# Performance work log

Measured on AMD Instinct MI355X. Metric: run time of the kernel, lower is better.

Reference implementation:

```python
import jax, jax.numpy as jnp
import numpy as np

N_WIN = 7    # n_win hardcoded in AR_Attention
TOPK = 4     # topk routing windows
HEADS = 8    # num_heads


def setup_inputs() -> dict:
    key = jax.random.key(0)
    ks = jax.random.split(key, 6)
    B, H, W, C = 4, 56, 56, 256
    s = 0.02
    x = jax.random.normal(ks[0], (B, H, W, C), jnp.float32)
    Wqkv = jax.random.normal(ks[1], (C, 3 * C), jnp.float32) * s  # Linear(dim, 3*dim) (qk_dim=dim)
    bqkv = jnp.zeros((3 * C,), jnp.float32)
    Wo = jax.random.normal(ks[2], (C, C), jnp.float32) * s        # output projection Linear(dim, dim)
    bo = jnp.zeros((C,), jnp.float32)
    lepe_w = jax.random.normal(ks[3], (5, 5, 1, C), jnp.float32) * s  # 5x5 depthwise conv (side_dwconv=5)
    lepe_b = jnp.zeros((C,), jnp.float32)
    return {"x": x, "Wqkv": Wqkv, "bqkv": bqkv, "Wo": Wo, "bo": bo,
            "lepe_w": lepe_w, "lepe_b": lepe_b}


def reference(x, Wqkv, bqkv, Wo, bo, lepe_w, lepe_b):
    B, H, W, C = x.shape
    nw = N_WIN
    h, w = H // nw, W // nw           # region size (8x8)
    p2 = nw * nw                      # number of regions (49)
    hd = C // HEADS                   # head dim
    scale = float(C) ** -0.5          # qk_scale = qk_dim ** -0.5 (qk_dim = dim)

    # region partition: [B,H,W,C] -> [B,p2,h,w,C]
    xr = x.reshape(B, nw, h, nw, w, C).transpose(0, 1, 3, 2, 4, 5).reshape(B, p2, h, w, C)

    qkv = xr @ Wqkv + bqkv            # [B,p2,h,w,3C]
    q, kv = qkv[..., :C], qkv[..., C:]

    q_pix = q.reshape(B, p2, h * w, C)
    kv_pix = kv.reshape(B, p2, h * w, 2 * C)   # kv_downsample_mode='identity'

    # region-level queries/keys via per-window mean pooling
    q_win = q.mean((2, 3))                     # [B,p2,C]
    k_win = kv[..., :C].mean((2, 3))           # [B,p2,C]

    # LEPE: 5x5 depthwise conv on v over the full image grid
    v_img = kv[..., C:].reshape(B, nw, nw, h, w, C).transpose(0, 1, 3, 2, 4, 5).reshape(B, H, W, C)
    lepe = jax.lax.conv_general_dilated(
        v_img, lepe_w, (1, 1), 'SAME',
        dimension_numbers=('NHWC', 'HWIO', 'NHWC'),
        feature_group_count=C) + lepe_b

    # top-k window routing (param_routing=False, hard routing, mul_weight='none')
    r_logit = jnp.einsum('bpc,bqc->bpq', q_win * scale, k_win)  # [B,p2,p2]
    _, r_idx = jax.lax.top_k(r_logit, TOPK)                     # [B,p2,TOPK]

    # gather selected kv windows: [B,p2,TOPK,h*w,2C]
    kv_sel = jax.vmap(lambda kvp, i: kvp[i])(kv_pix, r_idx)

    k_sel = kv_sel[..., :C].reshape(B, p2, TOPK * h * w, HEADS, hd)
    v_sel = kv_sel[..., C:].reshape(B, p2, TOPK * h * w, HEADS, hd)
    qh = q_pix.reshape(B, p2, h * w, HEADS, hd)

    attn = jnp.einsum('bpqnd,bpknd->bpnqk', qh * scale, k_sel)  # [B,p2,heads,hw,TOPK*hw]
    attn = jax.nn.softmax(attn, axis=-1)
    out = jnp.einsum('bpnqk,bpknd->bpqnd', attn, v_sel).reshape(B, p2, h, w, C)

    # windows back to image grid
    out = out.reshape(B, nw, nw, h, w, C).transpose(0, 1, 3, 2, 4, 5).reshape(B, H, W, C)
    out = out + lepe
    return out @ Wo + bo
```

## Files before the change

### kernel.cpp

```cpp
#include <hip/hip_runtime.h>
#include <hip/hip_bf16.h>

#define NPIX 12544

typedef short bf16x8 __attribute__((ext_vector_type(8)));
typedef float f32x4  __attribute__((ext_vector_type(4)));

__device__ __forceinline__ float bf2f(unsigned short u) {
    unsigned int x = ((unsigned int)u) << 16;
    float f; __builtin_memcpy(&f, &x, sizeof(f)); return f;
}
__device__ __forceinline__ unsigned short f2bf(float f) {
    __hip_bfloat16 h = __float2bfloat16(f);
    unsigned short u; __builtin_memcpy(&u, &h, 2); return u;
}
__device__ __forceinline__ void load_lds16(const unsigned short* g, unsigned short* l) {
    __builtin_amdgcn_global_load_lds(
        (const __attribute__((address_space(1))) unsigned int*)g,
        (__attribute__((address_space(3))) unsigned int*)l,
        16, 0, 0);
}

__global__ __launch_bounds__(256) void k_prep(
    const float* __restrict__ X, unsigned short* __restrict__ Xb,
    float* __restrict__ xmean,
    const float* __restrict__ Wqkv, const float* __restrict__ Wo,
    unsigned short* __restrict__ Wtq, unsigned short* __restrict__ Wto)
{
    __shared__ __align__(16) unsigned char sm[64 * 65 * 4];
    const int t = threadIdx.x;
    const int blk = blockIdx.x;
    if (blk < 392) {
        float* part = (float*)sm;
        const int w = blk >> 1, hc = blk & 1;
        const int b = w / 49, p = w % 49;
        const int wi = p / 7, wj = p % 7;
        const int ch0 = hc * 128;
        const int ps = t >> 5, cg = t & 31;
        float4 s = {0.f, 0.f, 0.f, 0.f};
        #pragma unroll
        for (int i = 0; i < 8; i++) {
            int pp = ps * 8 + i;
            int y = wi * 8 + (pp >> 3), x = wj * 8 + (pp & 7);
            int idx = (((b * 56) + y) * 56 + x) * 256 + ch0 + cg * 4;
            float4 v = *reinterpret_cast<const float4*>(X + idx);
            s.x += v.x; s.y += v.y; s.z += v.z; s.w += v.w;
            ushort4 o = { f2bf(v.x), f2bf(v.y), f2bf(v.z), f2bf(v.w) };
            *reinterpret_cast<ushort4*>(Xb + idx) = o;
        }
        *reinterpret_cast<float4*>(part + t * 4) = *reinterpret_cast<float4*>(&s);
        __syncthreads();
        if (t < 32) {
            float4 m = {0.f, 0.f, 0.f, 0.f};
            #pragma unroll
            for (int ps2 = 0; ps2 < 8; ps2++) {
                float4 v = *reinterpret_cast<float4*>(part + (ps2 * 32 + t) * 4);
                m.x += v.x; m.y += v.y; m.z += v.z; m.w += v.w;
            }
            m.x *= (1.f / 64.f); m.y *= (1.f / 64.f);
            m.z *= (1.f / 64.f); m.w *= (1.f / 64.f);
            *reinterpret_cast<float4*>(xmean + w * 256 + ch0 + t * 4) = m;
        }
    } else {
        float* tile = (float*)sm;
        int tb = blk - 392;
        const float* Wsrc; unsigned short* Wdst; int N, kt, nt;
        if (tb < 48) { Wsrc = Wqkv; Wdst = Wtq; N = 768; kt = tb / 12; nt = tb % 12; }
        else { tb -= 48; Wsrc = Wo; Wdst = Wto; N = 256; kt = tb / 4; nt = tb % 4; }
        const int k0 = kt * 64, n0 = nt * 64;
        const int r0 = t >> 6, c = t & 63;
        #pragma unroll
        for (int i = 0; i < 16; i++) {
            int r = i * 4 + r0;
            tile[r * 65 + c] = Wsrc[(size_t)(k0 + r) * N + n0 + c];
        }
        __syncthreads();
        #pragma unroll
        for (int i = 0; i < 16; i++) {
            int n = i * 4 + r0;
            Wdst[(size_t)(n0 + n) * 256 + k0 + c] = f2bf(tile[c * 65 + n]);
        }
    }
}

__global__ __launch_bounds__(256) void k_main1(
    const unsigned short* __restrict__ A,
    const unsigned short* __restrict__ Bt,
    const float* __restrict__ bias,
    unsigned short* __restrict__ O,
    const float* __restrict__ xmean,
    const float* __restrict__ Wqkv,
    float* __restrict__ qwin, float* __restrict__ kwin)
{
    __shared__ __align__(16) unsigned char sm1[16384];
    const int t = threadIdx.x;
    const int blk = blockIdx.x;
    if (blk < 588) {
        unsigned short* As = (unsigned short*)sm1;
        unsigned short* Bs = (unsigned short*)(sm1 + 8192);
        const int m0 = (blk % 98) * 128, n0 = (blk / 98) * 128;
        const int wave = t >> 6, lane = t & 63, quad = lane >> 4, lo = lane & 15;
        const int wm = wave & 1, wn = wave >> 1;
        const int sr = wave * 16 + (lane >> 2);
        const int sc = lane & 3;
        f32x4 acc[4][4];
        #pragma unroll
        for (int i = 0; i < 4; i++)
            #pragma unroll
            for (int j = 0; j < 4; j++) acc[i][j] = (f32x4){0.f, 0.f, 0.f, 0.f};

        for (int kt = 0; kt < 256; kt += 32) {
            __syncthreads();
            #pragma unroll
            for (int j = 0; j < 2; j++) {
                int row = j * 64 + sr;
                int e = sc ^ ((row >> 1) & 3);
                load_lds16(A  + (size_t)(m0 + row) * 256 + kt + e * 8, &As[row * 32 + sc * 8]);
                load_lds16(Bt + (size_t)(n0 + row) * 256 + kt + e * 8, &Bs[row * 32 + sc * 8]);
            }
            __syncthreads();
            bf16x8 af[4], bfr[4];
            #pragma unroll
            for (int mt = 0; mt < 4; mt++) {
                int row = wm * 64 + mt * 16 + lo;
                int c = quad ^ ((row >> 1) & 3);
                af[mt] = *reinterpret_cast<const bf16x8*>(&As[row * 32 + c * 8]);
            }
            #pragma unroll
            for (int nt = 0; nt < 4; nt++) {
                int col = wn * 64 + nt * 16 + lo;
                int c = quad ^ ((col >> 1) & 3);
                bfr[nt] = *reinterpret_cast<const bf16x8*>(&Bs[col * 32 + c * 8]);
            }
            #pragma unroll
            for (int mt = 0; mt < 4; mt++)
                #pragma unroll
                for (int nt = 0; nt < 4; nt++)
                    acc[mt][nt] = __builtin_amdgcn_mfma_f32_16x16x32_bf16(
                        af[mt], bfr[nt], acc[mt][nt], 0, 0, 0);
        }
        float bv[4];
        #pragma unroll
        for (int nt = 0; nt < 4; nt++) bv[nt] = bias[n0 + wn * 64 + nt * 16 + lo];
        #pragma unroll
        for (int mt = 0; mt < 4; mt++)
            #pragma unroll
            for (int nt = 0; nt < 4; nt++) {
                int n = n0 + wn * 64 + nt * 16 + lo;
                #pragma unroll
                for (int r = 0; r < 4; r++) {
                    int m = m0 + wm * 64 + mt * 16 + quad * 4 + r;
                    O[m * 768 + n] = f2bf(acc[mt][nt][r] + bv[nt]);
                }
            }
    } else {
        float* xs = (float*)sm1;
        const int u = blk - 588;
        const int bp = u % 196;
        const int half = u / 196;
        const int c = t;
        xs[c] = xmean[bp * 256 + c];
        __syncthreads();
        const int col = half * 256 + c;
        float a = 0.f;
        for (int k = 0; k < 256; k++) a += xs[k] * Wqkv[k * 768 + col];
        float* outp = half ? kwin : qwin;
        outp[bp * 256 + c] = a + bias[col];
    }
}

__global__ __launch_bounds__(256) void k_main2(
    const float* __restrict__ qwin, const float* __restrict__ kwin,
    int* __restrict__ ridx,
    const unsigned short* __restrict__ QKV,
    const float* __restrict__ lw, const float* __restrict__ lb,
    unsigned short* __restrict__ Olepe)
{
    __shared__ __align__(16) unsigned char sm2[25600];
    const int t = threadIdx.x;
    const int blk = blockIdx.x;
    if (blk < 196) {
        float* part = (float*)sm2;
        float* lg   = (float*)(sm2 + 49 * 4 * 4);
        const int b = blk / 49, p = blk % 49;
        if (t < 196) {
            int d = t >> 2, pr = t & 3;
            const float* qp = &qwin[(b * 49 + p) * 256];
            const float* kp = &kwin[(b * 49 + d) * 256];
            float a = 0.f;
            for (int ch = pr * 64; ch < pr * 64 + 64; ch++) a += qp[ch] * kp[ch];
            part[d * 4 + pr] = a;
        }
        __syncthreads();
        if (t < 49) lg[t] = part[t * 4 + 0] + part[t * 4 + 1] + part[t * 4 + 2] + part[t * 4 + 3];
        __syncthreads();
        if (t == 0) {
            unsigned long long used = 0ull;
            for (int sel = 0; sel < 4; sel++) {
                float best = -1e30f; int bi = 0;
                for (int qq = 0; qq < 49; qq++)
                    if (!((used >> qq) & 1ull) && lg[qq] > best) { best = lg[qq]; bi = qq; }
                used |= (1ull << bi);
                ridx[blk * 4 + sel] = bi;
            }
        }
    } else {
        float* lws = (float*)sm2;
        #pragma unroll
        for (int i = 0; i < 25; i++) lws[i * 256 + t] = lw[i * 256 + t];

        const int pl = t & 7;
        const int cg = t >> 3;
        const int c0 = cg * 8;
        const int gid = (blk - 196) * 8 + pl;
        const int b = gid / 3136, rem = gid % 3136;
        const int y = rem / 56, x = rem % 56;
        __syncthreads();

        float acc[8];
        {
            float4 b0 = *reinterpret_cast<const float4*>(lb + c0);
            float4 b1 = *reinterpret_cast<const float4*>(lb + c0 + 4);
            acc[0] = b0.x; acc[1] = b0.y; acc[2] = b0.z; acc[3] = b0.w;
            acc[4] = b1.x; acc[5] = b1.y; acc[6] = b1.z; acc[7] = b1.w;
        }
        #pragma unroll
        for (int ky = 0; ky < 5; ky++) {
            int yy = y + ky - 2;
            if (yy < 0 || yy >= 56) continue;
            #pragma unroll
            for (int kx = 0; kx < 5; kx++) {
                int xx = x + kx - 2;
                if (xx < 0 || xx >= 56) continue;
                bf16x8 v = *reinterpret_cast<const bf16x8*>(
                    QKV + (((b * 56) + yy) * 56 + xx) * 768 + 512 + c0);
                const float* wrow = &lws[(ky * 5 + kx) * 256 + c0];
                float4 w0 = *reinterpret_cast<const float4*>(wrow);
                float4 w1 = *reinterpret_cast<const float4*>(wrow + 4);
                acc[0] += bf2f((unsigned short)v[0]) * w0.x;
                acc[1] += bf2f((unsigned short)v[1]) * w0.y;
                acc[2] += bf2f((unsigned short)v[2]) * w0.z;
                acc[3] += bf2f((unsigned short)v[3]) * w0.w;
                acc[4] += bf2f((unsigned short)v[4]) * w1.x;
                acc[5] += bf2f((unsigned short)v[5]) * w1.y;
                acc[6] += bf2f((unsigned short)v[6]) * w1.z;
                acc[7] += bf2f((unsigned short)v[7]) * w1.w;
            }
        }
        bf16x8 o;
        #pragma unroll
        for (int j = 0; j < 8; j++) o[j] = (short)f2bf(acc[j]);
        *reinterpret_cast<bf16x8*>(Olepe + (size_t)gid * 256 + c0) = o;
    }
}

__global__ __launch_bounds__(256) void k_attn(
    const unsigned short* __restrict__ QKV,
    const int* __restrict__ ridx,
    const unsigned short* __restrict__ Olepe,
    unsigned short* __restrict__ Osum)
{
    __shared__ __align__(16) unsigned char smem[50688];
    unsigned short* Vt = (unsigned short*)smem;
    unsigned short* Qs = (unsigned short*)(smem + 16896);
    unsigned short* Ks = (unsigned short*)(smem + 22016);
    unsigned short* Ps = (unsigned short*)(smem + 16896);

    const int p = blockIdx.x, head = blockIdx.y, b = blockIdx.z;
    const int t = threadIdx.x;
    const int wi = p / 7, wj = p % 7;
    const int wave = t >> 6, lane = t & 63, quad = lane >> 4, lo = lane & 15;
    const int pix4 = t >> 2, c4 = t & 3;

    {
        int y = wi * 8 + (pix4 >> 3), x = wj * 8 + (pix4 & 7);
        const unsigned short* qp = QKV + (((b * 56) + y) * 56 + x) * 768 + head * 32 + c4 * 8;
        bf16x8 v = *reinterpret_cast<const bf16x8*>(qp);
        int sw = c4 ^ ((pix4 >> 3) & 3);
        *reinterpret_cast<bf16x8*>(&Qs[pix4 * 40 + sw * 8]) = v;
    }
    #pragma unroll
    for (int pass = 0; pass < 4; pass++) {
        int sel = ridx[(b * 49 + p) * 4 + pass];
        int si = sel / 7, sj = sel % 7;
        int y = si * 8 + (pix4 >> 3), x = sj * 8 + (pix4 & 7);
        const unsigned short* base = QKV + (((b * 56) + y) * 56 + x) * 768 + 256 + head * 32;
        bf16x8 kv = *reinterpret_cast<const bf16x8*>(base + c4 * 8);
        bf16x8 vv = *reinterpret_cast<const bf16x8*>(base + 256 + c4 * 8);
        int krow = pass * 64 + pix4;
        int sw = c4 ^ ((krow >> 3) & 3);
        *reinterpret_cast<bf16x8*>(&Ks[krow * 40 + sw * 8]) = kv;
        #pragma unroll
        for (int j = 0; j < 8; j++)
            Vt[(c4 * 8 + j) * 264 + krow] = (unsigned short)vv[j];
    }
    __syncthreads();

    f32x4 sc[16];
    {
        int row = wave * 16 + lo;
        bf16x8 af = *reinterpret_cast<const bf16x8*>(
            &Qs[row * 40 + ((quad ^ ((row >> 3) & 3)) * 8)]);
        f32x4 z = (f32x4){0.f, 0.f, 0.f, 0.f};
        #pragma unroll
        for (int nt = 0; nt < 16; nt++) {
            int key = nt * 16 + lo;
            bf16x8 bfr = *reinterpret_cast<const bf16x8*>(
                &Ks[key * 40 + ((quad ^ ((key >> 3) & 3)) * 8)]);
            sc[nt] = __builtin_amdgcn_mfma_f32_16x16x32_bf16(af, bfr, z, 0, 0, 0);
        }
    }
    float M[4] = {-1e30f, -1e30f, -1e30f, -1e30f};
    #pragma unroll
    for (int nt = 0; nt < 16; nt++)
        #pragma unroll
        for (int r = 0; r < 4; r++) M[r] = fmaxf(M[r], sc[nt][r] * 0.0625f);
    #pragma unroll
    for (int d = 1; d < 16; d <<= 1)
        #pragma unroll
        for (int r = 0; r < 4; r++) M[r] = fmaxf(M[r], __shfl_xor(M[r], d));
    float l[4] = {0.f, 0.f, 0.f, 0.f};
    #pragma unroll
    for (int nt = 0; nt < 16; nt++)
        #pragma unroll
        for (int r = 0; r < 4; r++) {
            float e = __expf(sc[nt][r] * 0.0625f - M[r]);
            sc[nt][r] = e;
            l[r] += e;
        }
    #pragma unroll
    for (int d = 1; d < 16; d <<= 1)
        #pragma unroll
        for (int r = 0; r < 4; r++) l[r] += __shfl_xor(l[r], d);

    __syncthreads();

    unsigned short* myPs = Ps + wave * 16 * 264;
    #pragma unroll
    for (int nt = 0; nt < 16; nt++)
        #pragma unroll
        for (int r = 0; r < 4; r++)
            myPs[(quad * 4 + r) * 264 + nt * 16 + lo] = f2bf(sc[nt][r]);

    f32x4 o0 = (f32x4){0.f, 0.f, 0.f, 0.f}, o1 = o0;
    #pragma unroll
    for (int kt = 0; kt < 8; kt++) {
        bf16x8 pa = *reinterpret_cast<const bf16x8*>(
            &myPs[lo * 264 + kt * 32 + quad * 8]);
        bf16x8 vb0 = *reinterpret_cast<const bf16x8*>(
            &Vt[lo * 264 + kt * 32 + quad * 8]);
        bf16x8 vb1 = *reinterpret_cast<const bf16x8*>(
            &Vt[(16 + lo) * 264 + kt * 32 + quad * 8]);
        o0 = __builtin_amdgcn_mfma_f32_16x16x32_bf16(pa, vb0, o0, 0, 0, 0);
        o1 = __builtin_amdgcn_mfma_f32_16x16x32_bf16(pa, vb1, o1, 0, 0, 0);
    }
    #pragma unroll
    for (int r = 0; r < 4; r++) {
        int q = wave * 16 + quad * 4 + r;
        int y = wi * 8 + (q >> 3), x = wj * 8 + (q & 7);
        size_t base = (size_t)(((b * 56) + y) * 56 + x) * 256 + head * 32;
        const unsigned short* lp = Olepe + base;
        unsigned short* op = Osum + base;
        float inv = 1.0f / l[r];
        op[lo]      = f2bf(o0[r] * inv + bf2f(lp[lo]));
        op[16 + lo] = f2bf(o1[r] * inv + bf2f(lp[16 + lo]));
    }
}

__global__ __launch_bounds__(256) void k_proj(
    const unsigned short* __restrict__ A,
    const unsigned short* __restrict__ Bt,
    const float* __restrict__ bias,
    float* __restrict__ O)
{
    __shared__ unsigned short As[128 * 32];
    __shared__ unsigned short Bs[64 * 32];
    const int t = threadIdx.x;
    const int m0 = blockIdx.x * 128, n0 = blockIdx.y * 64;
    const int wave = t >> 6, lane = t & 63, quad = lane >> 4, lo = lane & 15;
    const int sr = wave * 16 + (lane >> 2);
    const int sc = lane & 3;
    f32x4 acc[2][4];
    #pragma unroll
    for (int i = 0; i < 2; i++)
        #pragma unroll
        for (int j = 0; j < 4; j++) acc[i][j] = (f32x4){0.f, 0.f, 0.f, 0.f};

    for (int kt = 0; kt < 256; kt += 32) {
        __syncthreads();
        #pragma unroll
        for (int j = 0; j < 2; j++) {
            int row = j * 64 + sr;
            int e = sc ^ ((row >> 1) & 3);
            load_lds16(A + (size_t)(m0 + row) * 256 + kt + e * 8, &As[row * 32 + sc * 8]);
        }
        {
            int e = sc ^ ((sr >> 1) & 3);
            load_lds16(Bt + (size_t)(n0 + sr) * 256 + kt + e * 8, &Bs[sr * 32 + sc * 8]);
        }
        __syncthreads();
        bf16x8 af[2], bfr[4];
        #pragma unroll
        for (int mt = 0; mt < 2; mt++) {
            int row = wave * 32 + mt * 16 + lo;
            int c = quad ^ ((row >> 1) & 3);
            af[mt] = *reinterpret_cast<const bf16x8*>(&As[row * 32 + c * 8]);
        }
        #pragma unroll
        for (int nt = 0; nt < 4; nt++) {
            int col = nt * 16 + lo;
            int c = quad ^ ((col >> 1) & 3);
            bfr[nt] = *reinterpret_cast<const bf16x8*>(&Bs[col * 32 + c * 8]);
        }
        #pragma unroll
        for (int mt = 0; mt < 2; mt++)
            #pragma unroll
            for (int nt = 0; nt < 4; nt++)
                acc[mt][nt] = __builtin_amdgcn_mfma_f32_16x16x32_bf16(
                    af[mt], bfr[nt], acc[mt][nt], 0, 0, 0);
    }
    float bv[4];
    #pragma unroll
    for (int nt = 0; nt < 4; nt++) bv[nt] = bias[n0 + nt * 16 + lo];
    #pragma unroll
    for (int mt = 0; mt < 2; mt++)
        #pragma unroll
        for (int nt = 0; nt < 4; nt++) {
            int n = n0 + nt * 16 + lo;
            #pragma unroll
            for (int r = 0; r < 4; r++) {
                int m = m0 + wave * 32 + mt * 16 + quad * 4 + r;
                O[m * 256 + n] = acc[mt][nt][r] + bv[nt];
            }
        }
}

extern "C" void kernel_launch(void* const* d_in, const int* in_sizes, int n_in,
                              void* d_out, int out_size, void* d_ws, size_t ws_size,
                              hipStream_t stream)
{
    const float* x    = (const float*)d_in[0];
    const float* Wqkv = (const float*)d_in[1];
    const float* bqkv = (const float*)d_in[2];
    const float* Wo   = (const float*)d_in[3];
    const float* bo   = (const float*)d_in[4];
    const float* lw   = (const float*)d_in[5];
    const float* lb   = (const float*)d_in[6];
    float* out = (float*)d_out;

    char* ws = (char*)d_ws;
    size_t off = 0;
    unsigned short* qkv   = (unsigned short*)(ws + off); off += (size_t)NPIX * 768 * 2;
    unsigned short* xb    = (unsigned short*)(ws + off); off += (size_t)NPIX * 256 * 2;
    unsigned short* Wtq   = (unsigned short*)(ws + off); off += 768 * 256 * 2;
    unsigned short* Wto   = (unsigned short*)(ws + off); off += 256 * 256 * 2;
    unsigned short* Osum  = (unsigned short*)(ws + off); off += (size_t)NPIX * 256 * 2;
    unsigned short* Olepe = (unsigned short*)(ws + off); off += (size_t)NPIX * 256 * 2;
    float* xmean = (float*)(ws + off); off += 196 * 256 * 4;
    float* qwin  = (float*)(ws + off); off += 196 * 256 * 4;
    float* kwin  = (float*)(ws + off); off += 196 * 256 * 4;
    int*   ridx  = (int*)(ws + off);   off += 196 * 4 * 4;

    k_prep <<<dim3(456),      256, 0, stream>>>(x, xb, xmean, Wqkv, Wo, Wtq, Wto);
    k_main1<<<dim3(980),      256, 0, stream>>>(xb, Wtq, bqkv, qkv, xmean, Wqkv, qwin, kwin);
    k_main2<<<dim3(1764),     256, 0, stream>>>(qwin, kwin, ridx, qkv, lw, lb, Olepe);
    k_attn <<<dim3(49, 8, 4), 256, 0, stream>>>(qkv, ridx, Olepe, Osum);
    k_proj <<<dim3(98, 4),    256, 0, stream>>>(Osum, Wto, bo, out);
}
```

Baseline: 153.2 us.

## Fuse routing top-k into QKV GEMM kernel and LEPE conv into attention

Routing logits are now computed inside the QKV GEMM kernel's side blocks. Each block projects its window-mean query, folds it through the key weights into a per-query vector, and dots that with the window means of x, so per-window q/k means are never materialised. The 5x5 depthwise LEPE conv moves into the attention kernel: it stages a 12x12 halo of V per head in LDS and adds the result directly to the attention output. This removes one kernel launch and the Olepe and qwin/kwin global buffers and round-trips. In exchange the attention kernel does extra syncs and halo loads, and the LEPE weights are rounded to bf16.

```diff
diff --git a/kernel.cpp b/kernel.cpp
--- a/kernel.cpp
+++ b/kernel.cpp
@@ -90,7 +90,7 @@
     unsigned short* __restrict__ O,
     const float* __restrict__ xmean,
     const float* __restrict__ Wqkv,
-    float* __restrict__ qwin, float* __restrict__ kwin)
+    int* __restrict__ ridx)
 {
     __shared__ __align__(16) unsigned char sm1[16384];
     const int t = threadIdx.x;
@@ -154,45 +154,40 @@
                 }
             }
     } else {
-        float* xs = (float*)sm1;
+        float* xq   = (float*)sm1;
+        float* qs   = (float*)(sm1 + 1024);
+        float* us   = (float*)(sm1 + 2048);
+        float* part = (float*)(sm1 + 3072);
+        float* lg   = (float*)(sm1 + 3072 + 784);
         const int u = blk - 588;
-        const int bp = u % 196;
-        const int half = u / 196;
-        const int c = t;
-        xs[c] = xmean[bp * 256 + c];
-        __syncthreads();
-        const int col = half * 256 + c;
-        float a = 0.f;
-        for (int k = 0; k < 256; k++) a += xs[k] * Wqkv[k * 768 + col];
-        float* outp = half ? kwin : qwin;
-        outp[bp * 256 + c] = a + bias[col];
-    }
-}
-
-__global__ __launch_bounds__(256) void k_main2(
-    const float* __restrict__ qwin, const float* __restrict__ kwin,
-    int* __restrict__ ridx,
-    const unsigned short* __restrict__ QKV,
-    const float* __restrict__ lw, const float* __restrict__ lb,
-    unsigned short* __restrict__ Olepe)
-{
-    __shared__ __align__(16) unsigned char sm2[25600];
-    const int t = threadIdx.x;
-    const int blk = blockIdx.x;
-    if (blk < 196) {
-        float* part = (float*)sm2;
-        float* lg   = (float*)(sm2 + 49 * 4 * 4);
-        const int b = blk / 49, p = blk % 49;
+        const int b = u / 49;
+        xq[t] = xmean[(size_t)u * 256 + t];
+        __syncthreads();
+        {
+            float a = 0.f;
+            for (int k = 0; k < 256; k++) a += xq[k] * Wqkv[k * 768 + t];
+            qs[t] = a + bias[t];
+        }
+        __syncthreads();
+        {
+            const float* wr = Wqkv + (size_t)t * 768 + 256;
+            float a = 0.f;
+            for (int c = 0; c < 256; c += 4) {
+                float4 w = *reinterpret_cast<const float4*>(wr + c);
+                a += qs[c] * w.x + qs[c + 1] * w.y + qs[c + 2] * w.z + qs[c + 3] * w.w;
+            }
+            us[t] = a;
+        }
+        __syncthreads();
         if (t < 196) {
             int d = t >> 2, pr = t & 3;
-            const float* qp = &qwin[(b * 49 + p) * 256];
-            const float* kp = &kwin[(b * 49 + d) * 256];
+            const float* xm = xmean + (size_t)(b * 49 + d) * 256 + pr * 64;
             float a = 0.f;
-            for (int ch = pr * 64; ch < pr * 64 + 64; ch++) a += qp[ch] * kp[ch];
+            for (int k = 0; k < 64; k++) a += xm[k] * us[pr * 64 + k];
             part[d * 4 + pr] = a;
         }
         __syncthreads();
-        if (t < 49) lg[t] = part[t * 4 + 0] + part[t * 4 + 1] + part[t * 4 + 2] + part[t * 4 + 3];
+        if (t < 49) lg[t] = part[t * 4] + part[t * 4 + 1] + part[t * 4 + 2] + part[t * 4 + 3];
         __syncthreads();
         if (t == 0) {
             unsigned long long used = 0ull;
@@ -201,63 +196,16 @@
                 for (int qq = 0; qq < 49; qq++)
                     if (!((used >> qq) & 1ull) && lg[qq] > best) { best = lg[qq]; bi = qq; }
                 used |= (1ull << bi);
-                ridx[blk * 4 + sel] = bi;
-            }
-        }
-    } else {
-        float* lws = (float*)sm2;
-        #pragma unroll
-        for (int i = 0; i < 25; i++) lws[i * 256 + t] = lw[i * 256 + t];
-
-        const int pl = t & 7;
-        const int cg = t >> 3;
-        const int c0 = cg * 8;
-        const int gid = (blk - 196) * 8 + pl;
-        const int b = gid / 3136, rem = gid % 3136;
-        const int y = rem / 56, x = rem % 56;
-        __syncthreads();
-
-        float acc[8];
-        {
-            float4 b0 = *reinterpret_cast<const float4*>(lb + c0);
-            float4 b1 = *reinterpret_cast<const float4*>(lb + c0 + 4);
-            acc[0] = b0.x; acc[1] = b0.y; acc[2] = b0.z; acc[3] = b0.w;
-            acc[4] = b1.x; acc[5] = b1.y; acc[6] = b1.z; acc[7] = b1.w;
-        }
-        #pragma unroll
-        for (int ky = 0; ky < 5; ky++) {
-            int yy = y + ky - 2;
-            if (yy < 0 || yy >= 56) continue;
-            #pragma unroll
-            for (int kx = 0; kx < 5; kx++) {
-                int xx = x + kx - 2;
-                if (xx < 0 || xx >= 56) continue;
-                bf16x8 v = *reinterpret_cast<const bf16x8*>(
-                    QKV + (((b * 56) + yy) * 56 + xx) * 768 + 512 + c0);
-                const float* wrow = &lws[(ky * 5 + kx) * 256 + c0];
-                float4 w0 = *reinterpret_cast<const float4*>(wrow);
-                float4 w1 = *reinterpret_cast<const float4*>(wrow + 4);
-                acc[0] += bf2f((unsigned short)v[0]) * w0.x;
-                acc[1] += bf2f((unsigned short)v[1]) * w0.y;
-                acc[2] += bf2f((unsigned short)v[2]) * w0.z;
-                acc[3] += bf2f((unsigned short)v[3]) * w0.w;
-                acc[4] += bf2f((unsigned short)v[4]) * w1.x;
-                acc[5] += bf2f((unsigned short)v[5]) * w1.y;
-                acc[6] += bf2f((unsigned short)v[6]) * w1.z;
-                acc[7] += bf2f((unsigned short)v[7]) * w1.w;
-            }
-        }
-        bf16x8 o;
-        #pragma unroll
-        for (int j = 0; j < 8; j++) o[j] = (short)f2bf(acc[j]);
-        *reinterpret_cast<bf16x8*>(Olepe + (size_t)gid * 256 + c0) = o;
+                ridx[u * 4 + sel] = bi;
+            }
+        }
     }
 }
 
 __global__ __launch_bounds__(256) void k_attn(
     const unsigned short* __restrict__ QKV,
     const int* __restrict__ ridx,
-    const unsigned short* __restrict__ Olepe,
+    const float* __restrict__ lw, const float* __restrict__ lb,
     unsigned short* __restrict__ Osum)
 {
     __shared__ __align__(16) unsigned char smem[50688];
@@ -354,16 +302,70 @@
         o0 = __builtin_amdgcn_mfma_f32_16x16x32_bf16(pa, vb0, o0, 0, 0, 0);
         o1 = __builtin_amdgcn_mfma_f32_16x16x32_bf16(pa, vb1, o1, 0, 0, 0);
     }
+
+    __syncthreads();
+    unsigned short* Vimg = (unsigned short*)smem;
+    unsigned short* lwsb = (unsigned short*)(smem + 16896);
+    unsigned short* lepb = (unsigned short*)(smem + 18496);
+    if (t < 200) {
+        int tap = t >> 3, c = (t & 7) * 4;
+        float4 w = *reinterpret_cast<const float4*>(lw + tap * 256 + head * 32 + c);
+        unsigned short* dst = &lwsb[tap * 32 + c];
+        dst[0] = f2bf(w.x); dst[1] = f2bf(w.y); dst[2] = f2bf(w.z); dst[3] = f2bf(w.w);
+    }
+    {
+        const int y0 = wi * 8 - 2, x0 = wj * 8 - 2;
+        #pragma unroll
+        for (int i = 0; i < 3; i++) {
+            int idx = i * 256 + t;
+            if (idx < 576) {
+                int pp = idx >> 2, cc = idx & 3;
+                int py = y0 + pp / 12, px = x0 + pp % 12;
+                bf16x8 v = (bf16x8){0, 0, 0, 0, 0, 0, 0, 0};
+                if (py >= 0 && py < 56 && px >= 0 && px < 56)
+                    v = *reinterpret_cast<const bf16x8*>(
+                        QKV + (((b * 56) + py) * 56 + px) * 768 + 512 + head * 32 + cc * 8);
+                *reinterpret_cast<bf16x8*>(&Vimg[pp * 40 + cc * 8]) = v;
+            }
+        }
+    }
+    __syncthreads();
+    {
+        const int qpix = t >> 2, cc = t & 3;
+        const int qy = qpix >> 3, qx = qpix & 7;
+        float accl[8];
+        float4 b0 = *reinterpret_cast<const float4*>(lb + head * 32 + cc * 8);
+        float4 b1 = *reinterpret_cast<const float4*>(lb + head * 32 + cc * 8 + 4);
+        accl[0] = b0.x; accl[1] = b0.y; accl[2] = b0.z; accl[3] = b0.w;
+        accl[4] = b1.x; accl[5] = b1.y; accl[6] = b1.z; accl[7] = b1.w;
+        #pragma unroll
+        for (int ky = 0; ky < 5; ky++)
+            #pragma unroll
+            for (int kx = 0; kx < 5; kx++) {
+                int pp = (qy + ky) * 12 + (qx + kx);
+                bf16x8 v = *reinterpret_cast<const bf16x8*>(&Vimg[pp * 40 + cc * 8]);
+                bf16x8 w = *reinterpret_cast<const bf16x8*>(&lwsb[(ky * 5 + kx) * 32 + cc * 8]);
+                #pragma unroll
+                for (int j = 0; j < 8; j++)
+                    accl[j] += bf2f((unsigned short)v[j]) * bf2f((unsigned short)w[j]);
+            }
+        bf16x8 o;
+        #pragma unroll
+        for (int j = 0; j < 8; j++) o[j] = (short)f2bf(accl[j]);
+        *reinterpret_cast<bf16x8*>(&lepb[qpix * 40 + cc * 8]) = o;
+    }
+    __syncthreads();
+
     #pragma unroll
     for (int r = 0; r < 4; r++) {
         int q = wave * 16 + quad * 4 + r;
         int y = wi * 8 + (q >> 3), x = wj * 8 + (q & 7);
-        size_t base = (size_t)(((b * 56) + y) * 56 + x) * 256 + head * 32;
-        const unsigned short* lp = Olepe + base;
-        unsigned short* op = Osum + base;
+        unsigned short* op = Osum + (size_t)(((b * 56) + y) * 56 + x) * 256 + head * 32;
         float inv = 1.0f / l[r];
-        op[lo]      = f2bf(o0[r] * inv + bf2f(lp[lo]));
-        op[16 + lo] = f2bf(o1[r] * inv + bf2f(lp[16 + lo]));
+        float le0 = bf2f(lepb[q * 40 + lo]);
+        float le1 = bf2f(lepb[q * 40 + 16 + lo]);
+        op[lo]      = f2bf(o0[r] * inv + le0);
+        op[16 + lo] = f2bf(o1[r] * inv + le1);
     }
 }
 
@@ -455,15 +457,11 @@
     unsigned short* Wtq   = (unsigned short*)(ws + off); off += 768 * 256 * 2;
     unsigned short* Wto   = (unsigned short*)(ws + off); off += 256 * 256 * 2;
     unsigned short* Osum  = (unsigned short*)(ws + off); off += (size_t)NPIX * 256 * 2;
-    unsigned short* Olepe = (unsigned short*)(ws + off); off += (size_t)NPIX * 256 * 2;
     float* xmean = (float*)(ws + off); off += 196 * 256 * 4;
-    float* qwin  = (float*)(ws + off); off += 196 * 256 * 4;
-    float* kwin  = (float*)(ws + off); off += 196 * 256 * 4;
     int*   ridx  = (int*)(ws + off);   off += 196 * 4 * 4;
 
     k_prep <<<dim3(456),      256, 0, stream>>>(x, xb, xmean, Wqkv, Wo, Wtq, Wto);
-    k_main1<<<dim3(980),      256, 0, stream>>>(xb, Wtq, bqkv, qkv, xmean, Wqkv, qwin, kwin);
-    k_main2<<<dim3(1764),     256, 0, stream>>>(qwin, kwin, ridx, qkv, lw, lb, Olepe);
-    k_attn <<<dim3(49, 8, 4), 256, 0, stream>>>(qkv, ridx, Olepe, Osum);
+    k_main1<<<dim3(784),      256, 0, stream>>>(xb, Wtq, bqkv, qkv, xmean, Wqkv, ridx);
+    k_attn <<<dim3(49, 8, 4), 256, 0, stream>>>(qkv, ridx, lw, lb, Osum);
     k_proj <<<dim3(98, 4),    256, 0, stream>>>(Osum, Wto, bo, out);
 }
```

After: 167.6 us. +9.4%, slower.

## Fold routing into QKV kernel, merge attention with LEPE, sum in projection

Applied to the files above, without the earlier changes.

Routing logits are now computed algebraically as xmean·(Wk^T q), using a transposed fp32 Wk copy written in prep. This lets the routing and top-k run inside the QKV GEMM launch instead of a separate kernel. Attention blocks are merged into the same launch as the LEPE conv, writing separate outputs. The projection GEMM loads both buffers and adds them on the fly. This removes one kernel launch and the serial dependency between LEPE and attention. In exchange the projection kernel reads twice the A data, adds bf16 rounding of the sum, and the routing blocks do more serial dot-product work per block.

```diff
diff --git a/kernel.cpp b/kernel.cpp
--- a/kernel.cpp
+++ b/kernel.cpp
@@ -25,7 +25,8 @@
     const float* __restrict__ X, unsigned short* __restrict__ Xb,
     float* __restrict__ xmean,
     const float* __restrict__ Wqkv, const float* __restrict__ Wo,
-    unsigned short* __restrict__ Wtq, unsigned short* __restrict__ Wto)
+    unsigned short* __restrict__ Wtq, unsigned short* __restrict__ Wto,
+    float* __restrict__ WkT)
 {
     __shared__ __align__(16) unsigned char sm[64 * 65 * 4];
     const int t = threadIdx.x;
@@ -75,10 +76,13 @@
             tile[r * 65 + c] = Wsrc[(size_t)(k0 + r) * N + n0 + c];
         }
         __syncthreads();
+        const bool isWk = (N == 768) && (n0 >= 256) && (n0 < 512);
         #pragma unroll
         for (int i = 0; i < 16; i++) {
             int n = i * 4 + r0;
-            Wdst[(size_t)(n0 + n) * 256 + k0 + c] = f2bf(tile[c * 65 + n]);
+            float v = tile[c * 65 + n];
+            Wdst[(size_t)(n0 + n) * 256 + k0 + c] = f2bf(v);
+            if (isWk) WkT[(size_t)(n0 + n - 256) * 256 + k0 + c] = v;
         }
     }
 }
@@ -90,7 +94,8 @@
     unsigned short* __restrict__ O,
     const float* __restrict__ xmean,
     const float* __restrict__ Wqkv,
-    float* __restrict__ qwin, float* __restrict__ kwin)
+    const float* __restrict__ WkT,
+    int* __restrict__ ridx)
 {
     __shared__ __align__(16) unsigned char sm1[16384];
     const int t = threadIdx.x;
@@ -154,45 +159,36 @@
                 }
             }
     } else {
-        float* xs = (float*)sm1;
+        float* xq   = (float*)sm1;
+        float* qs   = (float*)(sm1 + 1024);
+        float* us   = (float*)(sm1 + 2048);
+        float* part = (float*)(sm1 + 3072);
+        float* lg   = (float*)(sm1 + 3072 + 784);
         const int u = blk - 588;
-        const int bp = u % 196;
-        const int half = u / 196;
-        const int c = t;
-        xs[c] = xmean[bp * 256 + c];
-        __syncthreads();
-        const int col = half * 256 + c;
-        float a = 0.f;
-        for (int k = 0; k < 256; k++) a += xs[k] * Wqkv[k * 768 + col];
-        float* outp = half ? kwin : qwin;
-        outp[bp * 256 + c] = a + bias[col];
-    }
-}
-
-__global__ __launch_bounds__(256) void k_main2(
-    const float* __restrict__ qwin, const float* __restrict__ kwin,
-    int* __restrict__ ridx,
-    const unsigned short* __restrict__ QKV,
-    const float* __restrict__ lw, const float* __restrict__ lb,
-    unsigned short* __restrict__ Olepe)
-{
-    __shared__ __align__(16) unsigned char sm2[25600];
-    const int t = threadIdx.x;
-    const int blk = blockIdx.x;
-    if (blk < 196) {
-        float* part = (float*)sm2;
-        float* lg   = (float*)(sm2 + 49 * 4 * 4);
-        const int b = blk / 49, p = blk % 49;
+        const int b = u / 49;
+        xq[t] = xmean[(size_t)u * 256 + t];
+        __syncthreads();
+        {
+            float a = 0.f;
+            for (int k = 0; k < 256; k++) a += xq[k] * Wqkv[k * 768 + t];
+            qs[t] = a + bias[t];
+        }
+        __syncthreads();
+        {
+            float a = 0.f;
+            for (int j = 0; j < 256; j++) a += qs[j] * WkT[j * 256 + t];
+            us[t] = a;
+        }
+        __syncthreads();
         if (t < 196) {
             int d = t >> 2, pr = t & 3;
-            const float* qp = &qwin[(b * 49 + p) * 256];
-            const float* kp = &kwin[(b * 49 + d) * 256];
+            const float* xm = xmean + (size_t)(b * 49 + d) * 256 + pr * 64;
             float a = 0.f;
-            for (int ch = pr * 64; ch < pr * 64 + 64; ch++) a += qp[ch] * kp[ch];
+            for (int k = 0; k < 64; k++) a += xm[k] * us[pr * 64 + k];
             part[d * 4 + pr] = a;
         }
         __syncthreads();
-        if (t < 49) lg[t] = part[t * 4 + 0] + part[t * 4 + 1] + part[t * 4 + 2] + part[t * 4 + 3];
+        if (t < 49) lg[t] = part[t * 4] + part[t * 4 + 1] + part[t * 4 + 2] + part[t * 4 + 3];
         __syncthreads();
         if (t == 0) {
             unsigned long long used = 0ull;
@@ -201,18 +197,134 @@
                 for (int qq = 0; qq < 49; qq++)
                     if (!((used >> qq) & 1ull) && lg[qq] > best) { best = lg[qq]; bi = qq; }
                 used |= (1ull << bi);
-                ridx[blk * 4 + sel] = bi;
-            }
+                ridx[u * 4 + sel] = bi;
+            }
+        }
+    }
+}
+
+__global__ __launch_bounds__(256) void k_main2(
+    const unsigned short* __restrict__ QKV,
+    const int* __restrict__ ridx,
+    const float* __restrict__ lw, const float* __restrict__ lb,
+    unsigned short* __restrict__ Oattn,
+    unsigned short* __restrict__ Olepe)
+{
+    __shared__ __align__(16) unsigned char smem[50688];
+    const int t = threadIdx.x;
+    const int blk = blockIdx.x;
+    if (blk < 1568) {
+        unsigned short* Vt = (unsigned short*)smem;
+        unsigned short* Qs = (unsigned short*)(smem + 16896);
+        unsigned short* Ks = (unsigned short*)(smem + 22016);
+        unsigned short* Ps = (unsigned short*)(smem + 16896);
+
+        const int b = blk / 392, rem = blk % 392;
+        const int head = rem / 49, p = rem % 49;
+        const int wi = p / 7, wj = p % 7;
+        const int wave = t >> 6, lane = t & 63, quad = lane >> 4, lo = lane & 15;
+        const int pix4 = t >> 2, c4 = t & 3;
+
+        {
+            int y = wi * 8 + (pix4 >> 3), x = wj * 8 + (pix4 & 7);
+            const unsigned short* qp = QKV + (((b * 56) + y) * 56 + x) * 768 + head * 32 + c4 * 8;
+            bf16x8 v = *reinterpret_cast<const bf16x8*>(qp);
+            int sw = c4 ^ ((pix4 >> 3) & 3);
+            *reinterpret_cast<bf16x8*>(&Qs[pix4 * 40 + sw * 8]) = v;
+        }
+        #pragma unroll
+        for (int pass = 0; pass < 4; pass++) {
+            int sel = ridx[(b * 49 + p) * 4 + pass];
+            int si = sel / 7, sj = sel % 7;
+            int y = si * 8 + (pix4 >> 3), x = sj * 8 + (pix4 & 7);
+            const unsigned short* base = QKV + (((b * 56) + y) * 56 + x) * 768 + 256 + head * 32;
+            bf16x8 kv = *reinterpret_cast<const bf16x8*>(base + c4 * 8);
+            bf16x8 vv = *reinterpret_cast<const bf16x8*>(base + 256 + c4 * 8);
+            int krow = pass * 64 + pix4;
+            int sw = c4 ^ ((krow >> 3) & 3);
+            *reinterpret_cast<bf16x8*>(&Ks[krow * 40 + sw * 8]) = kv;
+            #pragma unroll
+            for (int j = 0; j < 8; j++)
+                Vt[(c4 * 8 + j) * 264 + krow] = (unsigned short)vv[j];
+        }
+        __syncthreads();
+
+        f32x4 sc[16];
+        {
+            int row = wave * 16 + lo;
+            bf16x8 af = *reinterpret_cast<const bf16x8*>(
+                &Qs[row * 40 + ((quad ^ ((row >> 3) & 3)) * 8)]);
+            f32x4 z = (f32x4){0.f, 0.f, 0.f, 0.f};
+            #pragma unroll
+            for (int nt = 0; nt < 16; nt++) {
+                int key = nt * 16 + lo;
+                bf16x8 bfr = *reinterpret_cast<const bf16x8*>(
+                    &Ks[key * 40 + ((quad ^ ((key >> 3) & 3)) * 8)]);
+                sc[nt] = __builtin_amdgcn_mfma_f32_16x16x32_bf16(af, bfr, z, 0, 0, 0);
+            }
+        }
+        float M[4] = {-1e30f, -1e30f, -1e30f, -1e30f};
+        #pragma unroll
+        for (int nt = 0; nt < 16; nt++)
+            #pragma unroll
+            for (int r = 0; r < 4; r++) M[r] = fmaxf(M[r], sc[nt][r] * 0.0625f);
+        #pragma unroll
+        for (int d = 1; d < 16; d <<= 1)
+            #pragma unroll
+            for (int r = 0; r < 4; r++) M[r] = fmaxf(M[r], __shfl_xor(M[r], d));
+        float l[4] = {0.f, 0.f, 0.f, 0.f};
+        #pragma unroll
+        for (int nt = 0; nt < 16; nt++)
+            #pragma unroll
+            for (int r = 0; r < 4; r++) {
+                float e = __expf(sc[nt][r] * 0.0625f - M[r]);
+                sc[nt][r] = e;
+                l[r] += e;
+            }
+        #pragma unroll
+        for (int d = 1; d < 16; d <<= 1)
+            #pragma unroll
+            for (int r = 0; r < 4; r++) l[r] += __shfl_xor(l[r], d);
+
+        __syncthreads();
+
+        unsigned short* myPs = Ps + wave * 16 * 264;
+        #pragma unroll
+        for (int nt = 0; nt < 16; nt++)
+            #pragma unroll
+            for (int r = 0; r < 4; r++)
+                myPs[(quad * 4 + r) * 264 + nt * 16 + lo] = f2bf(sc[nt][r]);
+
+        f32x4 o0 = (f32x4){0.f, 0.f, 0.f, 0.f}, o1 = o0;
+        #pragma unroll
+        for (int kt = 0; kt < 8; kt++) {
+            bf16x8 pa = *reinterpret_cast<const bf16x8*>(
+                &myPs[lo * 264 + kt * 32 + quad * 8]);
+            bf16x8 vb0 = *reinterpret_cast<const bf16x8*>(
+                &Vt[lo * 264 + kt * 32 + quad * 8]);
+            bf16x8 vb1 = *reinterpret_cast<const bf16x8*>(
+                &Vt[(16 + lo) * 264 + kt * 32 + quad * 8]);
+            o0 = __builtin_amdgcn_mfma_f32_16x16x32_bf16(pa, vb0, o0, 0, 0, 0);
+            o1 = __builtin_amdgcn_mfma_f32_16x16x32_bf16(pa, vb1, o1, 0, 0, 0);
+        }
+        #pragma unroll
+        for (int r = 0; r < 4; r++) {
+            int q = wave * 16 + quad * 4 + r;
+            int y = wi * 8 + (q >> 3), x = wj * 8 + (q & 7);
+            unsigned short* op = Oattn + (size_t)(((b * 56) + y) * 56 + x) * 256 + head * 32;
+            float inv = 1.0f / l[r];
+            op[lo]      = f2bf(o0[r] * inv);
+            op[16 + lo] = f2bf(o1[r] * inv);
         }
     } else {
-        float* lws = (float*)sm2;
+        float* lws = (float*)smem;
         #pragma unroll
         for (int i = 0; i < 25; i++) lws[i * 256 + t] = lw[i * 256 + t];
 
         const int pl = t & 7;
         const int cg = t >> 3;
         const int c0 = cg * 8;
-        const int gid = (blk - 196) * 8 + pl;
+        const int gid = (blk - 1568) * 8 + pl;
         const int b = gid / 3136, rem = gid % 3136;
         const int y = rem / 56, x = rem % 56;
         __syncthreads();
@@ -254,126 +366,15 @@
     }
 }
 
-__global__ __launch_bounds__(256) void k_attn(
-    const unsigned short* __restrict__ QKV,
-    const int* __restrict__ ridx,
-    const unsigned short* __restrict__ Olepe,
-    unsigned short* __restrict__ Osum)
-{
-    __shared__ __align__(16) unsigned char smem[50688];
-    unsigned short* Vt = (unsigned short*)smem;
-    unsigned short* Qs = (unsigned short*)(smem + 16896);
-    unsigned short* Ks = (unsigned short*)(smem + 22016);
-    unsigned short* Ps = (unsigned short*)(smem + 16896);
-
-    const int p = blockIdx.x, head = blockIdx.y, b = blockIdx.z;
-    const int t = threadIdx.x;
-    const int wi = p / 7, wj = p % 7;
-    const int wave = t >> 6, lane = t & 63, quad = lane >> 4, lo = lane & 15;
-    const int pix4 = t >> 2, c4 = t & 3;
-
-    {
-        int y = wi * 8 + (pix4 >> 3), x = wj * 8 + (pix4 & 7);
-        const unsigned short* qp = QKV + (((b * 56) + y) * 56 + x) * 768 + head * 32 + c4 * 8;
-        bf16x8 v = *reinterpret_cast<const bf16x8*>(qp);
-        int sw = c4 ^ ((pix4 >> 3) & 3);
-        *reinterpret_cast<bf16x8*>(&Qs[pix4 * 40 + sw * 8]) = v;
-    }
-    #pragma unroll
-    for (int pass = 0; pass < 4; pass++) {
-        int sel = ridx[(b * 49 + p) * 4 + pass];
-        int si = sel / 7, sj = sel % 7;
-        int y = si * 8 + (pix4 >> 3), x = sj * 8 + (pix4 & 7);
-        const unsigned short* base = QKV + (((b * 56) + y) * 56 + x) * 768 + 256 + head * 32;
-        bf16x8 kv = *reinterpret_cast<const bf16x8*>(base + c4 * 8);
-        bf16x8 vv = *reinterpret_cast<const bf16x8*>(base + 256 + c4 * 8);
-        int krow = pass * 64 + pix4;
-        int sw = c4 ^ ((krow >> 3) & 3);
-        *reinterpret_cast<bf16x8*>(&Ks[krow * 40 + sw * 8]) = kv;
-        #pragma unroll
-        for (int j = 0; j < 8; j++)
-            Vt[(c4 * 8 + j) * 264 + krow] = (unsigned short)vv[j];
-    }
-    __syncthreads();
-
-    f32x4 sc[16];
-    {
-        int row = wave * 16 + lo;
-        bf16x8 af = *reinterpret_cast<const bf16x8*>(
-            &Qs[row * 40 + ((quad ^ ((row >> 3) & 3)) * 8)]);
-        f32x4 z = (f32x4){0.f, 0.f, 0.f, 0.f};
-        #pragma unroll
-        for (int nt = 0; nt < 16; nt++) {
-            int key = nt * 16 + lo;
-            bf16x8 bfr = *reinterpret_cast<const bf16x8*>(
-                &Ks[key * 40 + ((quad ^ ((key >> 3) & 3)) * 8)]);
-            sc[nt] = __builtin_amdgcn_mfma_f32_16x16x32_bf16(af, bfr, z, 0, 0, 0);
-        }
-    }
-    float M[4] = {-1e30f, -1e30f, -1e30f, -1e30f};
-    #pragma unroll
-    for (int nt = 0; nt < 16; nt++)
-        #pragma unroll
-        for (int r = 0; r < 4; r++) M[r] = fmaxf(M[r], sc[nt][r] * 0.0625f);
-    #pragma unroll
-    for (int d = 1; d < 16; d <<= 1)
-        #pragma unroll
-        for (int r = 0; r < 4; r++) M[r] = fmaxf(M[r], __shfl_xor(M[r], d));
-    float l[4] = {0.f, 0.f, 0.f, 0.f};
-    #pragma unroll
-    for (int nt = 0; nt < 16; nt++)
-        #pragma unroll
-        for (int r = 0; r < 4; r++) {
-            float e = __expf(sc[nt][r] * 0.0625f - M[r]);
-            sc[nt][r] = e;
-            l[r] += e;
-        }
-    #pragma unroll
-    for (int d = 1; d < 16; d <<= 1)
-        #pragma unroll
-        for (int r = 0; r < 4; r++) l[r] += __shfl_xor(l[r], d);
-
-    __syncthreads();
-
-    unsigned short* myPs = Ps + wave * 16 * 264;
-    #pragma unroll
-    for (int nt = 0; nt < 16; nt++)
-        #pragma unroll
-        for (int r = 0; r < 4; r++)
-            myPs[(quad * 4 + r) * 264 + nt * 16 + lo] = f2bf(sc[nt][r]);
-
-    f32x4 o0 = (f32x4){0.f, 0.f, 0.f, 0.f}, o1 = o0;
-    #pragma unroll
-    for (int kt = 0; kt < 8; kt++) {
-        bf16x8 pa = *reinterpret_cast<const bf16x8*>(
-            &myPs[lo * 264 + kt * 32 + quad * 8]);
-        bf16x8 vb0 = *reinterpret_cast<const bf16x8*>(
-            &Vt[lo * 264 + kt * 32 + quad * 8]);
-        bf16x8 vb1 = *reinterpret_cast<const bf16x8*>(
-            &Vt[(16 + lo) * 264 + kt * 32 + quad * 8]);
-        o0 = __builtin_amdgcn_mfma_f32_16x16x32_bf16(pa, vb0, o0, 0, 0, 0);
-        o1 = __builtin_amdgcn_mfma_f32_16x16x32_bf16(pa, vb1, o1, 0, 0, 0);
-    }
-    #pragma unroll
-    for (int r = 0; r < 4; r++) {
-        int q = wave * 16 + quad * 4 + r;
-        int y = wi * 8 + (q >> 3), x = wj * 8 + (q & 7);
-        size_t base = (size_t)(((b * 56) + y) * 56 + x) * 256 + head * 32;
-        const unsigned short* lp = Olepe + base;
-        unsigned short* op = Osum + base;
-        float inv = 1.0f / l[r];
-        op[lo]      = f2bf(o0[r] * inv + bf2f(lp[lo]));
-        op[16 + lo] = f2bf(o1[r] * inv + bf2f(lp[16 + lo]));
-    }
-}
-
 __global__ __launch_bounds__(256) void k_proj(
-    const unsigned short* __restrict__ A,
+    const unsigned short* __restrict__ A1,
+    const unsigned short* __restrict__ A2,
     const unsigned short* __restrict__ Bt,
     const float* __restrict__ bias,
     float* __restrict__ O)
 {
-    __shared__ unsigned short As[128 * 32];
+    __shared__ unsigned short As1[128 * 32];
+    __shared__ unsigned short As2[128 * 32];
     __shared__ unsigned short Bs[64 * 32];
     const int t = threadIdx.x;
     const int m0 = blockIdx.x * 128, n0 = blockIdx.y * 64;
@@ -392,7 +393,8 @@
         for (int j = 0; j < 2; j++) {
             int row = j * 64 + sr;
             int e = sc ^ ((row >> 1) & 3);
-            load_lds16(A + (size_t)(m0 + row) * 256 + kt + e * 8, &As[row * 32 + sc * 8]);
+            load_lds16(A1 + (size_t)(m0 + row) * 256 + kt + e * 8, &As1[row * 32 + sc * 8]);
+            load_lds16(A2 + (size_t)(m0 + row) * 256 + kt + e * 8, &As2[row * 32 + sc * 8]);
         }
         {
             int e = sc ^ ((sr >> 1) & 3);
@@ -404,7 +406,11 @@
         for (int mt = 0; mt < 2; mt++) {
             int row = wave * 32 + mt * 16 + lo;
             int c = quad ^ ((row >> 1) & 3);
-            af[mt] = *reinterpret_cast<const bf16x8*>(&As[row * 32 + c * 8]);
+            bf16x8 a1 = *reinterpret_cast<const bf16x8*>(&As1[row * 32 + c * 8]);
+            bf16x8 a2 = *reinterpret_cast<const bf16x8*>(&As2[row * 32 + c * 8]);
+            #pragma unroll
+            for (int j = 0; j < 8; j++)
+                af[mt][j] = (short)f2bf(bf2f((unsigned short)a1[j]) + bf2f((unsigned short)a2[j]));
         }
         #pragma unroll
         for (int nt = 0; nt < 4; nt++) {
@@ -454,16 +460,14 @@
     unsigned short* xb    = (unsigned short*)(ws + off); off += (size_t)NPIX * 256 * 2;
     unsigned short* Wtq   = (unsigned short*)(ws + off); off += 768 * 256 * 2;
     unsigned short* Wto   = (unsigned short*)(ws + off); off += 256 * 256 * 2;
-    unsigned short* Osum  = (unsigned short*)(ws + off); off += (size_t)NPIX * 256 * 2;
+    unsigned short* Oattn = (unsigned short*)(ws + off); off += (size_t)NPIX * 256 * 2;
     unsigned short* Olepe = (unsigned short*)(ws + off); off += (size_t)NPIX * 256 * 2;
+    float* WkT   = (float*)(ws + off); off += 256 * 256 * 4;
     float* xmean = (float*)(ws + off); off += 196 * 256 * 4;
-    float* qwin  = (float*)(ws + off); off += 196 * 256 * 4;
-    float* kwin  = (float*)(ws + off); off += 196 * 256 * 4;
     int*   ridx  = (int*)(ws + off);   off += 196 * 4 * 4;
 
-    k_prep <<<dim3(456),      256, 0, stream>>>(x, xb, xmean, Wqkv, Wo, Wtq, Wto);
-    k_main1<<<dim3(980),      256, 0, stream>>>(xb, Wtq, bqkv, qkv, xmean, Wqkv, qwin, kwin);
-    k_main2<<<dim3(1764),     256, 0, stream>>>(qwin, kwin, ridx, qkv, lw, lb, Olepe);
-    k_attn <<<dim3(49, 8, 4), 256, 0, stream>>>(qkv, ridx, Olepe, Osum);
-    k_proj <<<dim3(98, 4),    256, 0, stream>>>(Osum, Wto, bo, out);
-}
+    k_prep <<<dim3(456),   256, 0, stream>>>(x, xb, xmean, Wqkv, Wo, Wtq, Wto, WkT);
+    k_main1<<<dim3(784),   256, 0, stream>>>(xb, Wtq, bqkv, qkv, xmean, Wqkv, WkT, ridx);
+    k_main2<<<dim3(3136),  256, 0, stream>>>(qkv, ridx, lw, lb, Oattn, Olepe);
+    k_proj <<<dim3(98, 4), 256, 0, stream>>>(Oattn, Olepe, Wto, bo, out);
+}
```

New measurement: 170.1 us. 1.11x slower.

## Shrink attention LDS footprint with direct-to-LDS loads and split P staging

Applied to the files above, without the earlier changes.

Q and K tiles are now loaded with global_load_lds directly into unpadded, XOR-swizzled LDS rows (stride 32 instead of 40), and the softmax probability buffer is staged in two halves of 128 keys rather than all 256 at once. Together these cut shared memory per block from about 50KB to about 37KB, which is meant to allow more resident blocks per CU and skip the register round-trip for Q/K. The cost is an extra __syncthreads between the two P·V halves and a different swizzle pattern that may change LDS bank conflicts.

```diff
diff --git a/kernel.cpp b/kernel.cpp
--- a/kernel.cpp
+++ b/kernel.cpp
@@ -260,10 +260,10 @@
     const unsigned short* __restrict__ Olepe,
     unsigned short* __restrict__ Osum)
 {
-    __shared__ __align__(16) unsigned char smem[50688];
+    __shared__ __align__(16) unsigned char smem[37376];
     unsigned short* Vt = (unsigned short*)smem;
     unsigned short* Qs = (unsigned short*)(smem + 16896);
-    unsigned short* Ks = (unsigned short*)(smem + 22016);
+    unsigned short* Ks = (unsigned short*)(smem + 20992);
     unsigned short* Ps = (unsigned short*)(smem + 16896);
 
     const int p = blockIdx.x, head = blockIdx.y, b = blockIdx.z;
@@ -274,22 +274,20 @@
 
     {
         int y = wi * 8 + (pix4 >> 3), x = wj * 8 + (pix4 & 7);
-        const unsigned short* qp = QKV + (((b * 56) + y) * 56 + x) * 768 + head * 32 + c4 * 8;
-        bf16x8 v = *reinterpret_cast<const bf16x8*>(qp);
-        int sw = c4 ^ ((pix4 >> 3) & 3);
-        *reinterpret_cast<bf16x8*>(&Qs[pix4 * 40 + sw * 8]) = v;
+        int e = c4 ^ ((pix4 >> 1) & 3);
+        load_lds16(QKV + (size_t)(((b * 56) + y) * 56 + x) * 768 + head * 32 + e * 8,
+                   &Qs[pix4 * 32 + c4 * 8]);
     }
     #pragma unroll
     for (int pass = 0; pass < 4; pass++) {
         int sel = ridx[(b * 49 + p) * 4 + pass];
         int si = sel / 7, sj = sel % 7;
         int y = si * 8 + (pix4 >> 3), x = sj * 8 + (pix4 & 7);
-        const unsigned short* base = QKV + (((b * 56) + y) * 56 + x) * 768 + 256 + head * 32;
-        bf16x8 kv = *reinterpret_cast<const bf16x8*>(base + c4 * 8);
+        const unsigned short* base = QKV + (size_t)(((b * 56) + y) * 56 + x) * 768 + 256 + head * 32;
+        int krow = pass * 64 + pix4;
+        int e = c4 ^ ((krow >> 1) & 3);
+        load_lds16(base + e * 8, &Ks[krow * 32 + c4 * 8]);
         bf16x8 vv = *reinterpret_cast<const bf16x8*>(base + 256 + c4 * 8);
-        int krow = pass * 64 + pix4;
-        int sw = c4 ^ ((krow >> 3) & 3);
-        *reinterpret_cast<bf16x8*>(&Ks[krow * 40 + sw * 8]) = kv;
         #pragma unroll
         for (int j = 0; j < 8; j++)
             Vt[(c4 * 8 + j) * 264 + krow] = (unsigned short)vv[j];
@@ -300,13 +298,13 @@
     {
         int row = wave * 16 + lo;
         bf16x8 af = *reinterpret_cast<const bf16x8*>(
-            &Qs[row * 40 + ((quad ^ ((row >> 3) & 3)) * 8)]);
+            &Qs[row * 32 + ((quad ^ ((row >> 1) & 3)) * 8)]);
         f32x4 z = (f32x4){0.f, 0.f, 0.f, 0.f};
         #pragma unroll
         for (int nt = 0; nt < 16; nt++) {
             int key = nt * 16 + lo;
             bf16x8 bfr = *reinterpret_cast<const bf16x8*>(
-                &Ks[key * 40 + ((quad ^ ((key >> 3) & 3)) * 8)]);
+                &Ks[key * 32 + ((quad ^ ((key >> 1) & 3)) * 8)]);
             sc[nt] = __builtin_amdgcn_mfma_f32_16x16x32_bf16(af, bfr, z, 0, 0, 0);
         }
     }
@@ -335,18 +333,18 @@
 
     __syncthreads();
 
-    unsigned short* myPs = Ps + wave * 16 * 264;
-    #pragma unroll
-    for (int nt = 0; nt < 16; nt++)
+    unsigned short* myPs = Ps + wave * 16 * 136;
+    f32x4 o0 = (f32x4){0.f, 0.f, 0.f, 0.f}, o1 = o0;
+
+    #pragma unroll
+    for (int nt = 0; nt < 8; nt++)
         #pragma unroll
         for (int r = 0; r < 4; r++)
-            myPs[(quad * 4 + r) * 264 + nt * 16 + lo] = f2bf(sc[nt][r]);
-
-    f32x4 o0 = (f32x4){0.f, 0.f, 0.f, 0.f}, o1 = o0;
-    #pragma unroll
-    for (int kt = 0; kt < 8; kt++) {
+            myPs[(quad * 4 + r) * 136 + nt * 16 + lo] = f2bf(sc[nt][r]);
+    #pragma unroll
+    for (int kt = 0; kt < 4; kt++) {
         bf16x8 pa = *reinterpret_cast<const bf16x8*>(
-            &myPs[lo * 264 + kt * 32 + quad * 8]);
+            &myPs[lo * 136 + kt * 32 + quad * 8]);
         bf16x8 vb0 = *reinterpret_cast<const bf16x8*>(
             &Vt[lo * 264 + kt * 32 + quad * 8]);
         bf16x8 vb1 = *reinterpret_cast<const bf16x8*>(
@@ -354,6 +352,25 @@
         o0 = __builtin_amdgcn_mfma_f32_16x16x32_bf16(pa, vb0, o0, 0, 0, 0);
         o1 = __builtin_amdgcn_mfma_f32_16x16x32_bf16(pa, vb1, o1, 0, 0, 0);
     }
+    __syncthreads();
+
+    #pragma unroll
+    for (int nt = 8; nt < 16; nt++)
+        #pragma unroll
+        for (int r = 0; r < 4; r++)
+            myPs[(quad * 4 + r) * 136 + (nt - 8) * 16 + lo] = f2bf(sc[nt][r]);
+    #pragma unroll
+    for (int kt = 4; kt < 8; kt++) {
+        bf16x8 pa = *reinterpret_cast<const bf16x8*>(
+            &myPs[lo * 136 + (kt - 4) * 32 + quad * 8]);
+        bf16x8 vb0 = *reinterpret_cast<const bf16x8*>(
+            &Vt[lo * 264 + kt * 32 + quad * 8]);
+        bf16x8 vb1 = *reinterpret_cast<const bf16x8*>(
+            &Vt[(16 + lo) * 264 + kt * 32 + quad * 8]);
+        o0 = __builtin_amdgcn_mfma_f32_16x16x32_bf16(pa, vb0, o0, 0, 0, 0);
+        o1 = __builtin_amdgcn_mfma_f32_16x16x32_bf16(pa, vb1, o1, 0, 0, 0);
+    }
+
     #pragma unroll
     for (int r = 0; r < 4; r++) {
         int q = wave * 16 + quad * 4 + r;
```

After: 155.6 us. About the same (+1.6%).
